# Performance work log

Measured on AMD Instinct MI355X. Metric: run time of the kernel, lower is better.

The kernel has to match this reference:

```python
import jax, jax.numpy as jnp
import numpy as np

ROPE_THETA = 10000.0


def _apply_rope(x, rot_dim):
    # lucidrains RotaryEmbedding: only first rot_dim channels are rotated,
    # freqs are interleave-repeated, rotate_half works on (d r=2) pairs.
    S = x.shape[-2]
    half = rot_dim // 2
    inv_freq = 1.0 / (ROPE_THETA ** (jnp.arange(0, rot_dim, 2, dtype=jnp.float32) / rot_dim))  # [half]
    pos = jnp.arange(S, dtype=jnp.float32)
    freqs = pos[:, None] * inv_freq[None, :]          # [S, half]
    freqs = jnp.repeat(freqs, 2, axis=-1)             # [S, rot_dim] interleaved
    cos = jnp.cos(freqs).astype(x.dtype)
    sin = jnp.sin(freqs).astype(x.dtype)
    xl, xr = x[..., :rot_dim], x[..., rot_dim:]
    xp = xl.reshape(*xl.shape[:-1], half, 2)
    x1, x2 = xp[..., 0], xp[..., 1]
    rot_half = jnp.stack([-x2, x1], axis=-1).reshape(xl.shape)
    return jnp.concatenate([xl * cos + rot_half * sin, xr], axis=-1)


def setup_inputs() -> dict:
    key = jax.random.key(0)
    ks = jax.random.split(key, 7)
    B, Sa, Se, d_audio, d_score = 4, 4096, 2048, 1024, 1024
    d_h = min(d_audio, d_score)
    return {
        "x_audio": jax.random.normal(ks[0], (B, Sa, d_audio), jnp.float32),
        "x_event": jax.random.normal(ks[1], (B, Se, d_score), jnp.float32),
        "event_padding_mask": jax.random.randint(ks[2], (B, Se), 0, 2) > 0,
        "W_q": jax.random.normal(ks[3], (d_h, d_audio), jnp.float32) * (d_audio ** -0.5),
        "b_q": jax.random.normal(ks[4], (d_h,), jnp.float32) * 0.02,
        "W_k": jax.random.normal(ks[5], (d_h, d_score), jnp.float32) * (d_score ** -0.5),
        "b_k": jax.random.normal(ks[6], (d_h,), jnp.float32) * 0.02,
    }


def reference(x_audio, x_event, event_padding_mask, W_q, b_q, W_k, b_k):
    d_h = W_q.shape[0]
    rot_dim = d_h // 2  # RotaryEmbedding(dim=d_h//2) -> partial rotary over first d_h//2 channels
    Q = jnp.einsum("bsd,hd->bsh", x_audio, W_q) + b_q
    K = jnp.einsum("bed,hd->beh", x_event, W_k) + b_k
    Q = _apply_rope(Q, rot_dim)
    K = _apply_rope(K, rot_dim)
    attn = jnp.einsum("bsh,beh->bse", Q, K)  # [B, S_audio, S_event]
    mask = event_padding_mask[:, None, :]     # [B, 1, S_event]
    attn = jnp.where(mask, attn, jnp.float32(-jnp.inf))
    return attn
```

## Files before the change

kernel.cpp:

```cpp
#include <hip/hip_runtime.h>
#include <hip/hip_bf16.h>
#include <cmath>

#define BATCH 4
#define SA 4096
#define SE 2048
#define DIM 1024
#define ROT 512

#define BM 128
#define BN 128
#define BK 32

#define MASK_SENTINEL (-1.0e30f)

using short8  = __attribute__((ext_vector_type(8))) short;
using floatx4 = __attribute__((ext_vector_type(4))) float;

#define RFREQ 0.0519051171f

__device__ __forceinline__ void gl_lds16(const void* g, void* l) {
    __builtin_amdgcn_global_load_lds(
        (const __attribute__((address_space(1))) unsigned int*)g,
        (__attribute__((address_space(3))) unsigned int*)l, 16, 0, 0);
}

__device__ __forceinline__ short bf16_of(float f) {
    __hip_bfloat16 h = __float2bfloat16(f);
    return *reinterpret_cast<short*>(&h);
}

__global__ __launch_bounds__(256) void probe_mask_kernel(
    const int* __restrict__ mask_i, int* __restrict__ flag)
{
    __shared__ int s_bad;
    if (threadIdx.x == 0) s_bad = 0;
    __syncthreads();
    int bad = 0;
    for (int i = threadIdx.x; i < 1024; i += 256) {
        int v = mask_i[i];
        bad |= (v != 0 && v != 1) ? 1 : 0;
    }
    if (bad) atomicOr(&s_bad, 1);
    __syncthreads();
    if (threadIdx.x == 0) *flag = s_bad ? 0 : 1;
}

__global__ __launch_bounds__(256) void cvt_bf16_kernel(
    const float* __restrict__ in, short* __restrict__ out, int n8)
{
    int i = blockIdx.x * 256 + threadIdx.x;
    if (i >= n8) return;
    const float4 f0 = ((const float4*)in)[2 * i];
    const float4 f1 = ((const float4*)in)[2 * i + 1];
    short8 o;
    o[0] = bf16_of(f0.x); o[1] = bf16_of(f0.y);
    o[2] = bf16_of(f0.z); o[3] = bf16_of(f0.w);
    o[4] = bf16_of(f1.x); o[5] = bf16_of(f1.y);
    o[6] = bf16_of(f1.z); o[7] = bf16_of(f1.w);
    ((short8*)out)[i] = o;
}

__global__ __launch_bounds__(256) void rope_table_kernel(float2* __restrict__ tab)
{
    const int i   = blockIdx.x * 256 + threadIdx.x;
    const int h2  = i >> 12;
    const int pos = i & 4095;
    const float inv = exp2f(-RFREQ * (float)h2);
    float s, c;
    sincosf((float)pos * inv, &s, &c);
    tab[i] = make_float2(c, s);
}

template <int MODE>
__device__ __forceinline__ void gemm_body(
    const short* __restrict__ A,
    const short* __restrict__ B,
    const float* __restrict__ bias,
    const float2* __restrict__ ct,
    const void*  __restrict__ maskp,
    const int*   __restrict__ flag,
    void* __restrict__ outp,
    int smask)
{
    __shared__ short lA[BM * BK];
    __shared__ short lB[BN * BK];

    const int tid  = threadIdx.x;
    const int wid  = tid >> 6;
    const int lane = tid & 63;

    const int nbx = gridDim.x, nby = gridDim.y;
    const int id  = blockIdx.x + nbx * (blockIdx.y + nby * blockIdx.z);
    const int cpx = (nbx * nby * gridDim.z) >> 3;
    const int swz = (id & 7) * cpx + (id >> 3);
    const int bx  = swz % nbx;
    const int byz = swz / nbx;
    const int by  = byz % nby;
    const int bz  = byz / nby;

    const int m0 = by * BM;
    const int n0 = bx * BN;

    const short* Ab = A;
    const short* Bb = B;
    if (MODE == 1) {
        Ab += (size_t)bz * SA * DIM;
        Bb += (size_t)bz * SE * DIM;
    }

    const int srow = lane >> 2;
    const int scol = (lane & 3) * 16;

    const char* gA0 = (const char*)Ab + (size_t)(m0 + 0 * 64 + wid * 16 + srow) * (DIM * 2) + scol;
    const char* gA1 = (const char*)Ab + (size_t)(m0 + 1 * 64 + wid * 16 + srow) * (DIM * 2) + scol;
    const char* gB0 = (const char*)Bb + (size_t)(n0 + 0 * 64 + wid * 16 + srow) * (DIM * 2) + scol;
    const char* gB1 = (const char*)Bb + (size_t)(n0 + 1 * 64 + wid * 16 + srow) * (DIM * 2) + scol;
    char* lA0 = (char*)lA + (0 * 64 + wid * 16 + srow) * 64 + scol;
    char* lA1 = (char*)lA + (1 * 64 + wid * 16 + srow) * 64 + scol;
    char* lB0 = (char*)lB + (0 * 64 + wid * 16 + srow) * 64 + scol;
    char* lB1 = (char*)lB + (1 * 64 + wid * 16 + srow) * 64 + scol;

    const int wm = (wid >> 1) * 64;
    const int wn = (wid & 1) * 64;
    const int fr = lane & 15;
    const int fk = (lane >> 4) * 8;

    int aoff[4], boff[4];
#pragma unroll
    for (int i = 0; i < 4; ++i) {
        aoff[i] = (wm + i * 16 + fr) * BK + fk;
        boff[i] = (wn + i * 16 + fr) * BK + fk;
    }

    floatx4 acc[4][4] = {};

    for (int k0 = 0; k0 < DIM; k0 += BK) {
        const size_t kb = (size_t)k0 * 2;
        __syncthreads();
        gl_lds16(gA0 + kb, lA0);
        gl_lds16(gA1 + kb, lA1);
        gl_lds16(gB0 + kb, lB0);
        gl_lds16(gB1 + kb, lB1);
        __syncthreads();

        short8 af[4], bf[4];
#pragma unroll
        for (int i = 0; i < 4; ++i) af[i] = *(const short8*)&lA[aoff[i]];
#pragma unroll
        for (int i = 0; i < 4; ++i) bf[i] = *(const short8*)&lB[boff[i]];
#pragma unroll
        for (int mi = 0; mi < 4; ++mi)
#pragma unroll
            for (int ni = 0; ni < 4; ++ni)
                acc[mi][ni] = __builtin_amdgcn_mfma_f32_16x16x32_bf16(
                    af[mi], bf[ni], acc[mi][ni], 0, 0, 0);
    }

    const int rrow = (lane >> 4) * 4;

    if (MODE == 0) {
        short* out = (short*)outp;
#pragma unroll
        for (int ni = 0; ni < 4; ++ni) {
            const int h = n0 + wn + ni * 16 + fr;
            const float bv  = bias[h];
            const bool rope = (h < ROT);
            const float sgn = (h & 1) ? 1.f : -1.f;
            const float2* ctrow = ct + ((size_t)(h >> 1) << 12);
#pragma unroll
            for (int mi = 0; mi < 4; ++mi) {
                const int rbase = m0 + wm + mi * 16 + rrow;
                const int pbase = rbase & smask;
                float2 cs[4];
                if (rope) {
#pragma unroll
                    for (int r = 0; r < 4; ++r) cs[r] = ctrow[pbase + r];
                }
#pragma unroll
                for (int r = 0; r < 4; ++r) {
                    float v = acc[mi][ni][r] + bv;
                    float p = __shfl_xor(v, 1);
                    if (rope) v = v * cs[r].x + sgn * p * cs[r].y;
                    out[(size_t)(rbase + r) * DIM + h] = bf16_of(v);
                }
            }
        }
    } else {
        float* out = (float*)outp + (size_t)bz * SA * SE;
        const int fl = *flag;
#pragma unroll
        for (int ni = 0; ni < 4; ++ni) {
            const int e = n0 + wn + ni * 16 + fr;
            int mk;
            if (fl) mk = ((const int*)maskp)[(size_t)bz * SE + e];
            else    mk = ((const unsigned char*)maskp)[(size_t)bz * SE + e];
#pragma unroll
            for (int mi = 0; mi < 4; ++mi) {
                const int rbase = m0 + wm + mi * 16 + rrow;
#pragma unroll
                for (int r = 0; r < 4; ++r) {
                    const float v = mk ? acc[mi][ni][r] : MASK_SENTINEL;
                    out[(size_t)(rbase + r) * SE + e] = v;
                }
            }
        }
    }
}

__global__ __launch_bounds__(256) void gemm_proj_kernel(
    const short* __restrict__ A, const short* __restrict__ B,
    const float* __restrict__ bias, const float2* __restrict__ ct,
    short* __restrict__ out, int smask)
{
    gemm_body<0>(A, B, bias, ct, nullptr, nullptr, out, smask);
}

__global__ __launch_bounds__(256) void gemm_attn_kernel(
    const short* __restrict__ Q, const short* __restrict__ K,
    const void* __restrict__ maskp, const int* __restrict__ flag,
    float* __restrict__ out)
{
    gemm_body<1>(Q, K, nullptr, nullptr, maskp, flag, out, 0);
}

extern "C" void kernel_launch(void* const* d_in, const int* in_sizes, int n_in,
                              void* d_out, int out_size, void* d_ws, size_t ws_size,
                              hipStream_t stream)
{
    const float* x_audio = (const float*)d_in[0];
    const float* x_event = (const float*)d_in[1];
    const void*  maskp   = d_in[2];
    const float* W_q     = (const float*)d_in[3];
    const float* b_q     = (const float*)d_in[4];
    const float* W_k     = (const float*)d_in[5];
    const float* b_k     = (const float*)d_in[6];
    float* out = (float*)d_out;

    char* ws = (char*)d_ws;
    short* xbf  = (short*)(ws);
    short* Qbf  = (short*)(ws + (size_t)32 * 1024 * 1024);
    short* Kbf  = (short*)(ws + (size_t)64 * 1024 * 1024);
    short* Wqbf = (short*)(ws + (size_t)80 * 1024 * 1024);
    short* Wkbf = (short*)(ws + (size_t)82 * 1024 * 1024);
    int*   flag = (int*)  (ws + (size_t)84 * 1024 * 1024);
    float2* ct  = (float2*)d_out;

    probe_mask_kernel<<<1, 256, 0, stream>>>((const int*)maskp, flag);
    rope_table_kernel<<<4096, 256, 0, stream>>>(ct);

    const int nxa8 = BATCH * SA * DIM / 8;
    const int nxe8 = BATCH * SE * DIM / 8;
    const int nw8  = DIM * DIM / 8;

    cvt_bf16_kernel<<<(nxa8 + 255) / 256, 256, 0, stream>>>(x_audio, xbf, nxa8);
    cvt_bf16_kernel<<<(nw8 + 255) / 256, 256, 0, stream>>>(W_q, Wqbf, nw8);
    gemm_proj_kernel<<<dim3(DIM / BN, (BATCH * SA) / BM, 1), 256, 0, stream>>>(
        xbf, Wqbf, b_q, ct, Qbf, SA - 1);

    cvt_bf16_kernel<<<(nxe8 + 255) / 256, 256, 0, stream>>>(x_event, xbf, nxe8);
    cvt_bf16_kernel<<<(nw8 + 255) / 256, 256, 0, stream>>>(W_k, Wkbf, nw8);
    gemm_proj_kernel<<<dim3(DIM / BN, (BATCH * SE) / BM, 1), 256, 0, stream>>>(
        xbf, Wkbf, b_k, ct, Kbf, SE - 1);

    gemm_attn_kernel<<<dim3(SE / BN, SA / BM, BATCH), 256, 0, stream>>>(
        Qbf, Kbf, maskp, flag, out);
}
```

Before: 408.8 us.

## Rewrite GEMMs as 256x256 tile, 8-wave, double-buffered swizzled-LDS pipeline

Replaces the 128x128x32 single-buffered GEMM with a 256x256 tile and K-step 64, computed by 512 threads (8 waves). It uses 128KB of LDS double-buffered with an XOR swizzle, and interleaves global-to-LDS prefetch of later K tiles with MFMA quadrants under fine-grained barriers and setprio. The aim is to raise data reuse, hide load latency and avoid LDS bank conflicts. In exchange it uses more registers and LDS, allows only one block per CU with 128KB LDS, and produces fewer blocks for the small projection grids.

```diff
diff --git a/kernel.cpp b/kernel.cpp
--- a/kernel.cpp
+++ b/kernel.cpp
@@ -7,10 +7,7 @@
 #define SE 2048
 #define DIM 1024
 #define ROT 512
-
-#define BM 128
-#define BN 128
-#define BK 32
+#define NT (DIM / 64)
 
 #define MASK_SENTINEL (-1.0e30f)
 
@@ -29,6 +26,8 @@
     __hip_bfloat16 h = __float2bfloat16(f);
     return *reinterpret_cast<short*>(&h);
 }
+
+__device__ __forceinline__ int imin(int a, int b) { return a < b ? a : b; }
 
 __global__ __launch_bounds__(256) void probe_mask_kernel(
     const int* __restrict__ mask_i, int* __restrict__ flag)
@@ -73,7 +72,7 @@
 }
 
 template <int MODE>
-__device__ __forceinline__ void gemm_body(
+__device__ __forceinline__ void gemm8_body(
     const short* __restrict__ A,
     const short* __restrict__ B,
     const float* __restrict__ bias,
@@ -83,8 +82,11 @@
     void* __restrict__ outp,
     int smask)
 {
-    __shared__ short lA[BM * BK];
-    __shared__ short lB[BN * BK];
+    __shared__ char smem[131072];
+    char* const lA0 = smem;
+    char* const lA1 = smem + 32768;
+    char* const lB0 = smem + 65536;
+    char* const lB1 = smem + 98304;
 
     const int tid  = threadIdx.x;
     const int wid  = tid >> 6;
@@ -93,14 +95,13 @@
     const int nbx = gridDim.x, nby = gridDim.y;
     const int id  = blockIdx.x + nbx * (blockIdx.y + nby * blockIdx.z);
     const int cpx = (nbx * nby * gridDim.z) >> 3;
-    const int swz = (id & 7) * cpx + (id >> 3);
-    const int bx  = swz % nbx;
-    const int byz = swz / nbx;
+    const int swzid = (id & 7) * cpx + (id >> 3);
+    const int bx  = swzid % nbx;
+    const int byz = swzid / nbx;
     const int by  = byz % nby;
     const int bz  = byz / nby;
-
-    const int m0 = by * BM;
-    const int n0 = bx * BN;
+    const int m0 = by * 256;
+    const int n0 = bx * 256;
 
     const short* Ab = A;
     const short* Bb = B;
@@ -109,53 +110,100 @@
         Bb += (size_t)bz * SE * DIM;
     }
 
-    const int srow = lane >> 2;
-    const int scol = (lane & 3) * 16;
-
-    const char* gA0 = (const char*)Ab + (size_t)(m0 + 0 * 64 + wid * 16 + srow) * (DIM * 2) + scol;
-    const char* gA1 = (const char*)Ab + (size_t)(m0 + 1 * 64 + wid * 16 + srow) * (DIM * 2) + scol;
-    const char* gB0 = (const char*)Bb + (size_t)(n0 + 0 * 64 + wid * 16 + srow) * (DIM * 2) + scol;
-    const char* gB1 = (const char*)Bb + (size_t)(n0 + 1 * 64 + wid * 16 + srow) * (DIM * 2) + scol;
-    char* lA0 = (char*)lA + (0 * 64 + wid * 16 + srow) * 64 + scol;
-    char* lA1 = (char*)lA + (1 * 64 + wid * 16 + srow) * 64 + scol;
-    char* lB0 = (char*)lB + (0 * 64 + wid * 16 + srow) * 64 + scol;
-    char* lB1 = (char*)lB + (1 * 64 + wid * 16 + srow) * 64 + scol;
-
-    const int wm = (wid >> 1) * 64;
-    const int wn = (wid & 1) * 64;
-    const int fr = lane & 15;
-    const int fk = (lane >> 4) * 8;
-
-    int aoff[4], boff[4];
-#pragma unroll
-    for (int i = 0; i < 4; ++i) {
-        aoff[i] = (wm + i * 16 + fr) * BK + fk;
-        boff[i] = (wn + i * 16 + fr) * BK + fk;
+    const int r8   = lane >> 3;
+    const int c16  = (lane & 7) << 4;
+    const int scs  = ((lane & 7) ^ r8) << 4;
+    const int arow = wid * 8 + r8;
+    const int brow = (wid & 3) * 8 + (wid >> 2) * 64 + r8;
+    const char* gA = (const char*)Ab + ((size_t)(m0 + arow) << 11) + scs;
+    const char* gB = (const char*)Bb + ((size_t)(n0 + brow) << 11) + scs;
+    const int ldsAt = arow * 128 + c16;
+    const int ldsBt = brow * 128 + c16;
+
+#define STG_A(dst, h, j, kt) \
+    gl_lds16(gA + (((size_t)((h)*64 + (j)*128) << 11) + (size_t)(kt)*128), \
+             (dst) + ((h)*64 + (j)*128) * 128 + ldsAt)
+#define STG_B(dst, h, j, kt) \
+    gl_lds16(gB + (((size_t)((h)*32 + (j)*128) << 11) + (size_t)(kt)*128), \
+             (dst) + ((h)*32 + (j)*128) * 128 + ldsBt)
+
+    const int fr  = lane & 15;
+    const int fq  = lane >> 4;
+    const int kc0 = (fq * 16) ^ ((fr & 7) << 4);
+    const int wm  = (wid >> 2) * 128;
+    const int wn  = (wid & 3) * 64;
+
+    floatx4 acc[8][4] = {};
+    short8 af[4][2];
+    short8 bfr[2][2][2];
+
+#define RD_A(lAc, mh) do {                                                   \
+    _Pragma("unroll") for (int mi4 = 0; mi4 < 4; ++mi4)                      \
+    _Pragma("unroll") for (int ks = 0; ks < 2; ++ks)                         \
+        af[mi4][ks] = *(const short8*)((lAc)                                 \
+            + (wm + (mh)*64 + mi4*16 + fr) * 128 + (kc0 ^ (ks*64)));         \
+} while (0)
+#define RD_B(lBc, nh) do {                                                   \
+    _Pragma("unroll") for (int ni2 = 0; ni2 < 2; ++ni2)                      \
+    _Pragma("unroll") for (int ks = 0; ks < 2; ++ks)                         \
+        bfr[nh][ni2][ks] = *(const short8*)((lBc)                            \
+            + (wn + (nh)*32 + ni2*16 + fr) * 128 + (kc0 ^ (ks*64)));         \
+} while (0)
+#define QUAD(mh, nh) do {                                                    \
+    __builtin_amdgcn_s_setprio(1);                                           \
+    _Pragma("unroll") for (int mi4 = 0; mi4 < 4; ++mi4)                      \
+    _Pragma("unroll") for (int ni2 = 0; ni2 < 2; ++ni2)                      \
+    _Pragma("unroll") for (int ks = 0; ks < 2; ++ks)                         \
+        acc[(mh)*4 + mi4][(nh)*2 + ni2] =                                    \
+            __builtin_amdgcn_mfma_f32_16x16x32_bf16(                         \
+                af[mi4][ks], bfr[nh][ni2][ks],                               \
+                acc[(mh)*4 + mi4][(nh)*2 + ni2], 0, 0, 0);                   \
+    __builtin_amdgcn_s_setprio(0);                                           \
+} while (0)
+#define BAR() do { __builtin_amdgcn_s_barrier();                             \
+                   __builtin_amdgcn_sched_barrier(0); } while (0)
+#define WAITV(n) asm volatile("s_waitcnt vmcnt(" #n ")" ::: "memory")
+
+    STG_A(lA0, 0, 0, 0); STG_A(lA0, 0, 1, 0);
+    STG_A(lA0, 1, 0, 0); STG_A(lA0, 1, 1, 0);
+    STG_B(lB0, 0, 0, 0); STG_B(lB0, 0, 1, 0);
+    STG_B(lB0, 1, 0, 0); STG_B(lB0, 1, 1, 0);
+    STG_A(lA1, 0, 0, 1); STG_A(lA1, 0, 1, 1);
+    STG_B(lB1, 0, 0, 1); STG_B(lB1, 0, 1, 1);
+    STG_A(lA1, 1, 0, 1); STG_A(lA1, 1, 1, 1);
+    WAITV(6);
+    BAR();
+
+    auto tile = [&](int t, char* lAc, char* lBc, char* lBn) {
+        const int kt1 = imin(t + 1, NT - 1);
+        const int kt2 = imin(t + 2, NT - 1);
+        RD_A(lAc, 0); RD_B(lBc, 0);
+        STG_B(lBn, 1, 0, kt1); STG_B(lBn, 1, 1, kt1);
+        BAR();
+        QUAD(0, 0);
+        BAR();
+        RD_B(lBc, 1);
+        STG_A(lAc, 0, 0, kt2); STG_A(lAc, 0, 1, kt2);
+        BAR();
+        QUAD(0, 1);
+        BAR();
+        RD_A(lAc, 1);
+        STG_B(lBc, 0, 0, kt2); STG_B(lBc, 0, 1, kt2);
+        BAR();
+        QUAD(1, 0);
+        BAR();
+        STG_A(lAc, 1, 0, kt2); STG_A(lAc, 1, 1, kt2);
+        BAR();
+        QUAD(1, 1);
+        WAITV(6);
+        BAR();
+    };
+
+    for (int t = 0; t < NT; t += 2) {
+        tile(t,     lA0, lB0, lB1);
+        tile(t + 1, lA1, lB1, lB0);
     }
-
-    floatx4 acc[4][4] = {};
-
-    for (int k0 = 0; k0 < DIM; k0 += BK) {
-        const size_t kb = (size_t)k0 * 2;
-        __syncthreads();
-        gl_lds16(gA0 + kb, lA0);
-        gl_lds16(gA1 + kb, lA1);
-        gl_lds16(gB0 + kb, lB0);
-        gl_lds16(gB1 + kb, lB1);
-        __syncthreads();
-
-        short8 af[4], bf[4];
-#pragma unroll
-        for (int i = 0; i < 4; ++i) af[i] = *(const short8*)&lA[aoff[i]];
-#pragma unroll
-        for (int i = 0; i < 4; ++i) bf[i] = *(const short8*)&lB[boff[i]];
-#pragma unroll
-        for (int mi = 0; mi < 4; ++mi)
-#pragma unroll
-            for (int ni = 0; ni < 4; ++ni)
-                acc[mi][ni] = __builtin_amdgcn_mfma_f32_16x16x32_bf16(
-                    af[mi], bf[ni], acc[mi][ni], 0, 0, 0);
-    }
+    WAITV(0);
 
     const int rrow = (lane >> 4) * 4;
 
@@ -169,7 +217,7 @@
             const float sgn = (h & 1) ? 1.f : -1.f;
             const float2* ctrow = ct + ((size_t)(h >> 1) << 12);
 #pragma unroll
-            for (int mi = 0; mi < 4; ++mi) {
+            for (int mi = 0; mi < 8; ++mi) {
                 const int rbase = m0 + wm + mi * 16 + rrow;
                 const int pbase = rbase & smask;
                 float2 cs[4];
@@ -196,7 +244,7 @@
             if (fl) mk = ((const int*)maskp)[(size_t)bz * SE + e];
             else    mk = ((const unsigned char*)maskp)[(size_t)bz * SE + e];
 #pragma unroll
-            for (int mi = 0; mi < 4; ++mi) {
+            for (int mi = 0; mi < 8; ++mi) {
                 const int rbase = m0 + wm + mi * 16 + rrow;
 #pragma unroll
                 for (int r = 0; r < 4; ++r) {
@@ -206,22 +254,29 @@
             }
         }
     }
-}
-
-__global__ __launch_bounds__(256) void gemm_proj_kernel(
+#undef STG_A
+#undef STG_B
+#undef RD_A
+#undef RD_B
+#undef QUAD
+#undef BAR
+#undef WAITV
+}
+
+__global__ __launch_bounds__(512, 2) void gemm8_proj_kernel(
     const short* __restrict__ A, const short* __restrict__ B,
     const float* __restrict__ bias, const float2* __restrict__ ct,
     short* __restrict__ out, int smask)
 {
-    gemm_body<0>(A, B, bias, ct, nullptr, nullptr, out, smask);
-}
-
-__global__ __launch_bounds__(256) void gemm_attn_kernel(
+    gemm8_body<0>(A, B, bias, ct, nullptr, nullptr, out, smask);
+}
+
+__global__ __launch_bounds__(512, 2) void gemm8_attn_kernel(
     const short* __restrict__ Q, const short* __restrict__ K,
     const void* __restrict__ maskp, const int* __restrict__ flag,
     float* __restrict__ out)
 {
-    gemm_body<1>(Q, K, nullptr, nullptr, maskp, flag, out, 0);
+    gemm8_body<1>(Q, K, nullptr, nullptr, maskp, flag, out, 0);
 }
 
 extern "C" void kernel_launch(void* const* d_in, const int* in_sizes, int n_in,
@@ -255,14 +310,14 @@
 
     cvt_bf16_kernel<<<(nxa8 + 255) / 256, 256, 0, stream>>>(x_audio, xbf, nxa8);
     cvt_bf16_kernel<<<(nw8 + 255) / 256, 256, 0, stream>>>(W_q, Wqbf, nw8);
-    gemm_proj_kernel<<<dim3(DIM / BN, (BATCH * SA) / BM, 1), 256, 0, stream>>>(
+    gemm8_proj_kernel<<<dim3(DIM / 256, (BATCH * SA) / 256, 1), 512, 0, stream>>>(
         xbf, Wqbf, b_q, ct, Qbf, SA - 1);
 
     cvt_bf16_kernel<<<(nxe8 + 255) / 256, 256, 0, stream>>>(x_event, xbf, nxe8);
     cvt_bf16_kernel<<<(nw8 + 255) / 256, 256, 0, stream>>>(W_k, Wkbf, nw8);
-    gemm_proj_kernel<<<dim3(DIM / BN, (BATCH * SE) / BM, 1), 256, 0, stream>>>(
+    gemm8_proj_kernel<<<dim3(DIM / 256, (BATCH * SE) / 256, 1), 512, 0, stream>>>(
         xbf, Wkbf, b_k, ct, Kbf, SE - 1);
 
-    gemm_attn_kernel<<<dim3(SE / BN, SA / BM, BATCH), 256, 0, stream>>>(
+    gemm8_attn_kernel<<<dim3(SE / 256, SA / 256, BATCH), 512, 0, stream>>>(
         Qbf, Kbf, maskp, flag, out);
 }
```

Measured after the change: 405.9 us. No clear change (-0.7%).

## Triple-buffer LDS with async prefetch, larger BM tile, and XOR swizzle

Applied to the files above, without the earlier changes.

Replaces the single-buffered LDS GEMM loop with a three-slab ring. Tile t+2 is prefetched via global_load_lds while tile t is computed, using explicit vmcnt waits and raw barriers, plus s_setprio around the MFMAs. It also doubles BM to 256 so each wave holds 8x4 accumulators, and XOR-swizzles the LDS layout to cut bank conflicts. The intent is to hide global-load latency and raise MFMA reuse, at the cost of more registers, 72KB of LDS per block and a fixed launch-bounds occupancy of 2.

```diff
diff --git a/kernel.cpp b/kernel.cpp
--- a/kernel.cpp
+++ b/kernel.cpp
@@ -8,9 +8,11 @@
 #define DIM 1024
 #define ROT 512
 
-#define BM 128
+#define BM 256
 #define BN 128
 #define BK 32
+#define NT (DIM / BK)
+#define SLAB 24576
 
 #define MASK_SENTINEL (-1.0e30f)
 
@@ -29,6 +31,8 @@
     __hip_bfloat16 h = __float2bfloat16(f);
     return *reinterpret_cast<short*>(&h);
 }
+
+__device__ __forceinline__ int imin(int a, int b) { return a < b ? a : b; }
 
 __global__ __launch_bounds__(256) void probe_mask_kernel(
     const int* __restrict__ mask_i, int* __restrict__ flag)
@@ -83,8 +87,10 @@
     void* __restrict__ outp,
     int smask)
 {
-    __shared__ short lA[BM * BK];
-    __shared__ short lB[BN * BK];
+    __shared__ char smem[3 * SLAB];
+    char* const s0 = smem;
+    char* const s1 = smem + SLAB;
+    char* const s2 = smem + 2 * SLAB;
 
     const int tid  = threadIdx.x;
     const int wid  = tid >> 6;
@@ -93,12 +99,11 @@
     const int nbx = gridDim.x, nby = gridDim.y;
     const int id  = blockIdx.x + nbx * (blockIdx.y + nby * blockIdx.z);
     const int cpx = (nbx * nby * gridDim.z) >> 3;
-    const int swz = (id & 7) * cpx + (id >> 3);
-    const int bx  = swz % nbx;
-    const int byz = swz / nbx;
+    const int swzid = (id & 7) * cpx + (id >> 3);
+    const int bx  = swzid % nbx;
+    const int byz = swzid / nbx;
     const int by  = byz % nby;
     const int bz  = byz / nby;
-
     const int m0 = by * BM;
     const int n0 = bx * BN;
 
@@ -109,55 +114,76 @@
         Bb += (size_t)bz * SE * DIM;
     }
 
-    const int srow = lane >> 2;
-    const int scol = (lane & 3) * 16;
-
-    const char* gA0 = (const char*)Ab + (size_t)(m0 + 0 * 64 + wid * 16 + srow) * (DIM * 2) + scol;
-    const char* gA1 = (const char*)Ab + (size_t)(m0 + 1 * 64 + wid * 16 + srow) * (DIM * 2) + scol;
-    const char* gB0 = (const char*)Bb + (size_t)(n0 + 0 * 64 + wid * 16 + srow) * (DIM * 2) + scol;
-    const char* gB1 = (const char*)Bb + (size_t)(n0 + 1 * 64 + wid * 16 + srow) * (DIM * 2) + scol;
-    char* lA0 = (char*)lA + (0 * 64 + wid * 16 + srow) * 64 + scol;
-    char* lA1 = (char*)lA + (1 * 64 + wid * 16 + srow) * 64 + scol;
-    char* lB0 = (char*)lB + (0 * 64 + wid * 16 + srow) * 64 + scol;
-    char* lB1 = (char*)lB + (1 * 64 + wid * 16 + srow) * 64 + scol;
-
-    const int wm = (wid >> 1) * 64;
+    const int srow  = lane >> 2;
+    const int sslot = lane & 3;
+    const int gsw   = ((sslot ^ (srow & 3)) << 4);
+    const char* gA = (const char*)Ab + (size_t)(m0 + wid * 16 + srow) * 2048 + gsw;
+    const char* gB = (const char*)Bb + (size_t)(n0 + wid * 16 + srow) * 2048 + gsw;
+    const int ldsT = (wid * 16 + srow) * 64 + sslot * 16;
+
+#define STG(slab, kt) do {                                                   \
+    gl_lds16(gA + 0 * 131072 + (size_t)(kt) * 64, (slab) + 0 * 4096 + ldsT); \
+    gl_lds16(gA + 1 * 131072 + (size_t)(kt) * 64, (slab) + 1 * 4096 + ldsT); \
+    gl_lds16(gA + 2 * 131072 + (size_t)(kt) * 64, (slab) + 2 * 4096 + ldsT); \
+    gl_lds16(gA + 3 * 131072 + (size_t)(kt) * 64, (slab) + 3 * 4096 + ldsT); \
+    gl_lds16(gB + 0 * 131072 + (size_t)(kt) * 64, (slab) + 16384 + ldsT);    \
+    gl_lds16(gB + 1 * 131072 + (size_t)(kt) * 64, (slab) + 20480 + ldsT);    \
+} while (0)
+
+    const int fr = lane & 15;
+    const int fq = lane >> 4;
+    const int ko = ((fq ^ (fr & 3)) << 4);
+    const int wm = (wid >> 1) * 128;
     const int wn = (wid & 1) * 64;
-    const int fr = lane & 15;
-    const int fk = (lane >> 4) * 8;
-
-    int aoff[4], boff[4];
-#pragma unroll
-    for (int i = 0; i < 4; ++i) {
-        aoff[i] = (wm + i * 16 + fr) * BK + fk;
-        boff[i] = (wn + i * 16 + fr) * BK + fk;
-    }
-
-    floatx4 acc[4][4] = {};
-
-    for (int k0 = 0; k0 < DIM; k0 += BK) {
-        const size_t kb = (size_t)k0 * 2;
-        __syncthreads();
-        gl_lds16(gA0 + kb, lA0);
-        gl_lds16(gA1 + kb, lA1);
-        gl_lds16(gB0 + kb, lB0);
-        gl_lds16(gB1 + kb, lB1);
-        __syncthreads();
-
-        short8 af[4], bf[4];
-#pragma unroll
-        for (int i = 0; i < 4; ++i) af[i] = *(const short8*)&lA[aoff[i]];
-#pragma unroll
-        for (int i = 0; i < 4; ++i) bf[i] = *(const short8*)&lB[boff[i]];
-#pragma unroll
-        for (int mi = 0; mi < 4; ++mi)
+
+    int aoff[8], boff[4];
+#pragma unroll
+    for (int mi = 0; mi < 8; ++mi) aoff[mi] = (wm + mi * 16 + fr) * 64 + ko;
+#pragma unroll
+    for (int ni = 0; ni < 4; ++ni) boff[ni] = 16384 + (wn + ni * 16 + fr) * 64 + ko;
+
+    floatx4 acc[8][4] = {};
+
+#define BAR() do { __builtin_amdgcn_s_barrier();                             \
+                   __builtin_amdgcn_sched_barrier(0); } while (0)
+#define WAITV(n) asm volatile("s_waitcnt vmcnt(" #n ")" ::: "memory")
+
+    STG(s0, 0);
+    STG(s1, 1);
+    WAITV(6);
+    BAR();
+
+    auto tile = [&](int t, char* cur, char* stg) {
+        const int kt2 = imin(t + 2, NT - 1);
+        short8 af[8], bfr[4];
+#pragma unroll
+        for (int mi = 0; mi < 8; ++mi) af[mi] = *(const short8*)(cur + aoff[mi]);
+#pragma unroll
+        for (int ni = 0; ni < 4; ++ni) bfr[ni] = *(const short8*)(cur + boff[ni]);
+        STG(stg, kt2);
+        BAR();
+        __builtin_amdgcn_s_setprio(1);
+#pragma unroll
+        for (int mi = 0; mi < 8; ++mi)
 #pragma unroll
             for (int ni = 0; ni < 4; ++ni)
                 acc[mi][ni] = __builtin_amdgcn_mfma_f32_16x16x32_bf16(
-                    af[mi], bf[ni], acc[mi][ni], 0, 0, 0);
-    }
-
-    const int rrow = (lane >> 4) * 4;
+                    af[mi], bfr[ni], acc[mi][ni], 0, 0, 0);
+        __builtin_amdgcn_s_setprio(0);
+        WAITV(6);
+        BAR();
+    };
+
+    for (int t = 0; t < NT - 2; t += 3) {
+        tile(t,     s0, s2);
+        tile(t + 1, s1, s0);
+        tile(t + 2, s2, s1);
+    }
+    tile(NT - 2, s0, s2);
+    tile(NT - 1, s1, s0);
+    WAITV(0);
+
+    const int rrow = fq * 4;
 
     if (MODE == 0) {
         short* out = (short*)outp;
@@ -169,7 +195,7 @@
             const float sgn = (h & 1) ? 1.f : -1.f;
             const float2* ctrow = ct + ((size_t)(h >> 1) << 12);
 #pragma unroll
-            for (int mi = 0; mi < 4; ++mi) {
+            for (int mi = 0; mi < 8; ++mi) {
                 const int rbase = m0 + wm + mi * 16 + rrow;
                 const int pbase = rbase & smask;
                 float2 cs[4];
@@ -196,7 +222,7 @@
             if (fl) mk = ((const int*)maskp)[(size_t)bz * SE + e];
             else    mk = ((const unsigned char*)maskp)[(size_t)bz * SE + e];
 #pragma unroll
-            for (int mi = 0; mi < 4; ++mi) {
+            for (int mi = 0; mi < 8; ++mi) {
                 const int rbase = m0 + wm + mi * 16 + rrow;
 #pragma unroll
                 for (int r = 0; r < 4; ++r) {
@@ -206,9 +232,12 @@
             }
         }
     }
-}
-
-__global__ __launch_bounds__(256) void gemm_proj_kernel(
+#undef STG
+#undef BAR
+#undef WAITV
+}
+
+__global__ __launch_bounds__(256, 2) void gemm_proj_kernel(
     const short* __restrict__ A, const short* __restrict__ B,
     const float* __restrict__ bias, const float2* __restrict__ ct,
     short* __restrict__ out, int smask)
@@ -216,7 +245,7 @@
     gemm_body<0>(A, B, bias, ct, nullptr, nullptr, out, smask);
 }
 
-__global__ __launch_bounds__(256) void gemm_attn_kernel(
+__global__ __launch_bounds__(256, 2) void gemm_attn_kernel(
     const short* __restrict__ Q, const short* __restrict__ K,
     const void* __restrict__ maskp, const int* __restrict__ flag,
     float* __restrict__ out)
```

After: 396.6 us. 1.03x faster.
